# Optimization experiments

Hardware: AMD Instinct MI355X
Metric: run time of the kernel (lower is better)

Reference implementation:

```python
import jax, jax.numpy as jnp
import numpy as np

N, E, IN_DIM, HIDDEN, OUT_DIM, HOPS, NUM_GRAPHS = 50000, 800000, 128, 128, 10, 4, 128


def setup_inputs() -> dict:
    key = jax.random.key(0)
    ks = jax.random.split(key, 10)
    x = jax.random.normal(ks[0], (N, IN_DIM), dtype=jnp.float32)
    edge_index = jax.random.randint(ks[1], (2, E), 0, N, dtype=jnp.int64)
    batch = jnp.sort(jax.random.randint(ks[2], (N,), 0, NUM_GRAPHS, dtype=jnp.int64))
    s = 0.05
    W_in = jax.random.normal(ks[3], (IN_DIM, HIDDEN), dtype=jnp.float32) * s
    b_in = jnp.zeros((HIDDEN,), dtype=jnp.float32)
    W_hops = jax.random.normal(ks[4], (HOPS, HIDDEN, HIDDEN), dtype=jnp.float32) * s
    b_hops = jnp.zeros((HOPS, HIDDEN), dtype=jnp.float32)
    W_cls = jax.random.normal(ks[5], (HIDDEN, OUT_DIM), dtype=jnp.float32) * s
    b_cls = jnp.zeros((OUT_DIM,), dtype=jnp.float32)
    return {"x": x, "edge_index": edge_index, "batch": batch,
            "W_in": W_in, "b_in": b_in, "W_hops": W_hops, "b_hops": b_hops,
            "W_cls": W_cls, "b_cls": b_cls}


def reference(x, edge_index, batch, W_in, b_in, W_hops, b_hops, W_cls, b_cls):
    src, dst = edge_index[0], edge_index[1]
    # LinearEncoder
    h = x @ W_in + b_in
    # GCN symmetric normalization with self-loops (edge weight 1):
    # deg[i] = 1 + in-degree(i)
    deg = 1.0 + jax.ops.segment_sum(jnp.ones((E,), h.dtype), dst, num_segments=N)
    dinv = deg ** -0.5                      # [N]
    edge_norm = (dinv[src] * dinv[dst])[:, None]   # [E,1]
    self_norm = (dinv * dinv)[:, None]             # [N,1]

    def gcn_conv(h, W, b):
        xw = h @ W                                           # [N,H]
        msg = xw[src] * edge_norm                            # gather + scale
        agg = jax.ops.segment_sum(msg, dst, num_segments=N)  # scatter-add
        return agg + xw * self_norm + b

    for i in range(HOPS):
        h = gcn_conv(h, W_hops[i], b_hops[i])
        if i != HOPS - 1:
            h = jax.nn.relu(h)  # dropout is identity in eval mode

    y = h @ W_cls + b_cls                                    # [N,OUT]
    # global mean pool over graphs
    sums = jax.ops.segment_sum(y, batch, num_segments=NUM_GRAPHS)
    cnts = jax.ops.segment_sum(jnp.ones((N,), y.dtype), batch, num_segments=NUM_GRAPHS)
    return sums / jnp.maximum(cnts, 1.0)[:, None]
```

## Files before the change

### kernel.cpp

```cpp
#include <hip/hip_runtime.h>
#include <hip/hip_fp16.h>

#define N_NODES 50000
#define N_EDGES 800000
#define HID 128
#define OUTD 10
#define NGRAPH 128
#define CAP 64
#define OVF_MAX 4096
#define GBM 64
#define EPT 2

typedef __attribute__((ext_vector_type(8))) short short8;
typedef __attribute__((ext_vector_type(4))) float f32x4;

__device__ __forceinline__ int ld_idx(const int* p, int i, int is64) {
  return is64 ? p[2 * i] : p[i];
}

__device__ __forceinline__ void split1(float v, unsigned& hb, unsigned& lb) {
  unsigned u = __float_as_uint(v);
  hb = (u + 0x7FFFu + ((u >> 16) & 1u)) >> 16;
  float r = v - __uint_as_float(hb << 16);
  unsigned ur = __float_as_uint(r);
  lb = (ur + 0x7FFFu + ((ur >> 16) & 1u)) >> 16;
}

__device__ __forceinline__ float4 h4_to_f4(uint2 u) {
  __half2 a = *(__half2*)&u.x;
  __half2 b = *(__half2*)&u.y;
  float2 fa = __half22float2(a);
  float2 fb = __half22float2(b);
  return make_float4(fa.x, fa.y, fb.x, fb.y);
}

__global__ __launch_bounds__(256) void setup_kernel(const int* __restrict__ ei,
                                                    const float* __restrict__ W_in,
                                                    const float* __restrict__ W_hops,
                                                    const float* __restrict__ Wc,
                                                    const float* __restrict__ b4,
                                                    const float* __restrict__ bc,
                                                    int* __restrict__ flag,
                                                    unsigned short* __restrict__ WhiT,
                                                    unsigned short* __restrict__ WloT,
                                                    float* __restrict__ Wf,
                                                    float* __restrict__ bf) {
  int b = blockIdx.x;
  int tid = threadIdx.x;
  if (b == 0) {
    if (tid == 0) {
      int all0 = 1;
      for (int i = 0; i < 64; ++i) {
        if (ei[2 * i + 1] != 0) { all0 = 0; break; }
      }
      flag[0] = all0;
    }
  } else if (b <= 4) {
    int m = b - 1;
    const float* W = (m == 0) ? W_in : (W_hops + (size_t)(m - 1) * HID * HID);
    unsigned short* oh = WhiT + (size_t)m * HID * HID;
    unsigned short* ol = WloT + (size_t)m * HID * HID;
    for (int it = 0; it < 64; ++it) {
      int idx = it * 256 + tid;
      int k = idx >> 7, n = idx & 127;
      unsigned hb, lb;
      split1(W[k * HID + n], hb, lb);
      oh[n * HID + k] = (unsigned short)hb;
      ol[n * HID + k] = (unsigned short)lb;
    }
  } else {
    const float* W4 = W_hops + 3 * (size_t)HID * HID;
    for (int idx = tid; idx < HID * OUTD; idx += 256) {
      int k = idx / OUTD, o = idx % OUTD;
      float s = 0.f;
      for (int j = 0; j < HID; ++j) s += W4[k * HID + j] * Wc[j * OUTD + o];
      Wf[idx] = s;
    }
    if (tid < OUTD) {
      float s = bc[tid];
      for (int j = 0; j < HID; ++j) s += b4[j] * Wc[j * OUTD + tid];
      bf[tid] = s;
    }
  }
}

template <bool A16>
__device__ __forceinline__ void gemm_mfma_body(const void* __restrict__ Av,
                                               const unsigned short* __restrict__ WhT,
                                               const unsigned short* __restrict__ WlT,
                                               const float* __restrict__ bias,
                                               __half* __restrict__ C16,
                                               int M, int row0) {
  __shared__ unsigned short sBall[2 * 64 * HID];
  unsigned short* sBhi = sBall;
  unsigned short* sBlo = sBall + 64 * HID;
  int tid = threadIdx.x;
  int w = tid >> 6, lane = tid & 63;
  int m = lane & 15, kq = lane >> 4;
  int arow = min(row0 + w * 16 + m, M - 1);

  short8 AH[4], AL[4];
#pragma unroll
  for (int kc4 = 0; kc4 < 4; ++kc4) {
    float av[8];
    if (A16) {
      const __half* Ap = (const __half*)Av + (size_t)arow * HID + kq * 8;
      uint4 raw = *(const uint4*)(Ap + kc4 * 32);
      float4 f0 = h4_to_f4(make_uint2(raw.x, raw.y));
      float4 f1 = h4_to_f4(make_uint2(raw.z, raw.w));
      av[0] = f0.x; av[1] = f0.y; av[2] = f0.z; av[3] = f0.w;
      av[4] = f1.x; av[5] = f1.y; av[6] = f1.z; av[7] = f1.w;
    } else {
      const float* Ap = (const float*)Av + (size_t)arow * HID + kq * 8;
      float4 a0 = *(const float4*)(Ap + kc4 * 32);
      float4 a1 = *(const float4*)(Ap + kc4 * 32 + 4);
      av[0] = a0.x; av[1] = a0.y; av[2] = a0.z; av[3] = a0.w;
      av[4] = a1.x; av[5] = a1.y; av[6] = a1.z; av[7] = a1.w;
    }
#pragma unroll
    for (int i = 0; i < 8; ++i) {
      unsigned hb, lb;
      split1(av[i], hb, lb);
      AH[kc4][i] = (short)hb;
      AL[kc4][i] = (short)lb;
    }
  }

  f32x4 acc[8];
#pragma unroll
  for (int j = 0; j < 8; ++j) acc[j] = (f32x4){0.f, 0.f, 0.f, 0.f};

#pragma unroll
  for (int half = 0; half < 2; ++half) {
    if (half) __syncthreads();
#pragma unroll
    for (int it = 0; it < 8; ++it) {
      int f = it * 256 + tid;
      int mat = f >> 10;
      int ln = (f >> 4) & 63;
      int c = f & 15;
      int cs = c ^ (ln & 15);
      const unsigned short* src = (mat ? WlT : WhT) + (size_t)(half * 64 + ln) * HID + c * 8;
      unsigned short* dst = (mat ? sBlo : sBhi) + ln * HID + cs * 8;
      *(uint4*)dst = *(const uint4*)src;
    }
    __syncthreads();

#pragma unroll
    for (int kc4 = 0; kc4 < 4; ++kc4) {
      int kc = kc4 * 4 + kq;
      int cs = kc ^ m;
#pragma unroll
      for (int jl = 0; jl < 4; ++jl) {
        int ln = jl * 16 + m;
        short8 bhi = *(const short8*)&sBhi[ln * HID + cs * 8];
        short8 blo = *(const short8*)&sBlo[ln * HID + cs * 8];
        int j = half * 4 + jl;
        acc[j] = __builtin_amdgcn_mfma_f32_16x16x32_bf16(AH[kc4], bhi, acc[j], 0, 0, 0);
        acc[j] = __builtin_amdgcn_mfma_f32_16x16x32_bf16(AL[kc4], bhi, acc[j], 0, 0, 0);
        acc[j] = __builtin_amdgcn_mfma_f32_16x16x32_bf16(AH[kc4], blo, acc[j], 0, 0, 0);
      }
    }
  }

  __syncthreads();
  float* sC = (float*)sBall;
  int rloc = w * 16 + (lane >> 4) * 4;
#pragma unroll
  for (int j = 0; j < 8; ++j) {
    int col = j * 16 + m;
    float bv = bias ? bias[col] : 0.f;
#pragma unroll
    for (int r = 0; r < 4; ++r)
      sC[(rloc + r) * HID + col] = acc[j][r] + bv;
  }
  __syncthreads();
#pragma unroll
  for (int it = 0; it < 8; ++it) {
    int f = it * 256 + tid;
    int rr = f >> 5;
    int c4 = (f & 31) * 4;
    int grow = row0 + rr;
    if (grow < M) {
      float4 v = *(const float4*)&sC[rr * HID + c4];
      __half2 h0 = __floats2half2_rn(v.x, v.y);
      __half2 h1 = __floats2half2_rn(v.z, v.w);
      uint2 u;
      u.x = *(unsigned*)&h0;
      u.y = *(unsigned*)&h1;
      *(uint2*)(C16 + (size_t)grow * HID + c4) = u;
    }
  }
}

template <bool A16>
__global__ __launch_bounds__(256) void gemm_kernel(const void* __restrict__ A,
                                                   const unsigned short* __restrict__ WhT,
                                                   const unsigned short* __restrict__ WlT,
                                                   __half* __restrict__ C16, int M) {
  gemm_mfma_body<A16>(A, WhT, WlT, nullptr, C16, M, blockIdx.x * GBM);
}

__device__ __forceinline__ void fill_phase(const int* __restrict__ ei,
                                           int* __restrict__ fillcnt,
                                           int* __restrict__ col_fixed,
                                           int* __restrict__ ovf_cnt,
                                           int* __restrict__ ovf,
                                           const int* __restrict__ flag,
                                           int e0, int e1) {
  int is64 = flag[0];
  int tid = threadIdx.x;
  int base = e0 + blockIdx.x * (256 * EPT);
  int dsts[EPT], srcs[EPT], pos[EPT];
#pragma unroll
  for (int u = 0; u < EPT; ++u) {
    int e = base + u * 256 + tid;
    if (e < e1) {
      dsts[u] = ld_idx(ei, N_EDGES + e, is64);
      srcs[u] = ld_idx(ei, e, is64);
    } else {
      dsts[u] = -1; srcs[u] = 0;
    }
  }
#pragma unroll
  for (int u = 0; u < EPT; ++u)
    pos[u] = (dsts[u] >= 0) ? atomicAdd(&fillcnt[dsts[u]], 1) : 0;
#pragma unroll
  for (int u = 0; u < EPT; ++u) {
    if (dsts[u] >= 0) {
      if (pos[u] < CAP) {
        col_fixed[dsts[u] * CAP + pos[u]] = srcs[u];
      } else {
        int o = atomicAdd(ovf_cnt, 1);
        if (o < OVF_MAX) { ovf[2 * o] = dsts[u]; ovf[2 * o + 1] = srcs[u]; }
      }
    }
  }
}

template <bool A16>
__global__ __launch_bounds__(256) void gemm_fill_kernel(const void* __restrict__ A,
                                                        const unsigned short* __restrict__ WhT,
                                                        const unsigned short* __restrict__ WlT,
                                                        const float* __restrict__ bias,
                                                        __half* __restrict__ C16,
                                                        const int* __restrict__ ei,
                                                        int* __restrict__ fillcnt,
                                                        int* __restrict__ col_fixed,
                                                        int* __restrict__ ovf_cnt,
                                                        int* __restrict__ ovf,
                                                        const int* __restrict__ flag,
                                                        int e0, int e1) {
  if (blockIdx.x & 1) {
    fill_phase(ei, fillcnt, col_fixed, ovf_cnt, ovf, flag, e0, e1);
    gemm_mfma_body<A16>(A, WhT, WlT, bias, C16, N_NODES, blockIdx.x * GBM);
  } else {
    gemm_mfma_body<A16>(A, WhT, WlT, bias, C16, N_NODES, blockIdx.x * GBM);
    fill_phase(ei, fillcnt, col_fixed, ovf_cnt, ovf, flag, e0, e1);
  }
}

template <bool FIRST>
__global__ __launch_bounds__(256) void agg_kernel(const __half* __restrict__ xw,
                                                  const int* __restrict__ fillcnt,
                                                  const int* __restrict__ col_fixed,
                                                  float* __restrict__ ew,
                                                  const float* __restrict__ bias,
                                                  const int* __restrict__ ovf_cnt,
                                                  const int* __restrict__ ovf,
                                                  __half* __restrict__ out) {
  int wave = threadIdx.x >> 6;
  int lane = threadIdx.x & 63;
  int node = blockIdx.x * 4 + wave;
  if (node >= N_NODES) return;
  int g = lane >> 4;
  int q = lane & 15;

  const uint4* x4 = (const uint4*)xw;
  int deg = fillcnt[node];
  int m = min(deg, CAP);
  float dd = rsqrtf(1.0f + (float)deg);
  float acc[8];
#pragma unroll
  for (int i = 0; i < 8; ++i) acc[i] = 0.f;

  if (g == 0) {
    float sn = dd * dd;
    uint4 raw = x4[(size_t)node * 16 + q];
    float4 f0 = h4_to_f4(make_uint2(raw.x, raw.y));
    float4 f1 = h4_to_f4(make_uint2(raw.z, raw.w));
    float4 b0 = ((const float4*)bias)[2 * q];
    float4 b1 = ((const float4*)bias)[2 * q + 1];
    acc[0] = f0.x * sn + b0.x; acc[1] = f0.y * sn + b0.y;
    acc[2] = f0.z * sn + b0.z; acc[3] = f0.w * sn + b0.w;
    acc[4] = f1.x * sn + b1.x; acc[5] = f1.y * sn + b1.y;
    acc[6] = f1.z * sn + b1.z; acc[7] = f1.w * sn + b1.w;
  }

  int cidx = node;
  float cw = 0.f;
  if (lane < m) {
    cidx = col_fixed[node * CAP + lane];
    if (FIRST) {
      cw = rsqrtf(1.0f + (float)fillcnt[cidx]) * dd;
      ew[node * CAP + lane] = cw;
    } else {
      cw = ew[node * CAP + lane];
    }
  }

#define GFETCH(JJ, BUF, WB)                                                              \
  {                                                                                      \
    int _sg = min((JJ) + g, 63);                                                         \
    int _src = __builtin_amdgcn_ds_bpermute(_sg << 2, cidx);                             \
    WB = __uint_as_float((unsigned)__builtin_amdgcn_ds_bpermute(_sg << 2,                \
                                                                (int)__float_as_uint(cw))); \
    BUF = x4[(size_t)_src * 16 + q];                                                     \
  }

  if (m > 0) {
    uint4 b0, b1;
    float w0, w1;
    GFETCH(0, b0, w0);
    GFETCH(4, b1, w1);
    for (int jj = 0; jj < m; jj += 4) {
      const __half2* ph = (const __half2*)&b0;
#pragma unroll
      for (int t = 0; t < 4; ++t) {
        float2 f = __half22float2(ph[t]);
        acc[2 * t] = fmaf(f.x, w0, acc[2 * t]);
        acc[2 * t + 1] = fmaf(f.y, w0, acc[2 * t + 1]);
      }
      b0 = b1; w0 = w1;
      GFETCH(jj + 8, b1, w1);
    }
  }
#undef GFETCH

  if (deg > CAP && g == 0) {
    int novf = min(*ovf_cnt, OVF_MAX);
    for (int o = 0; o < novf; ++o) {
      if (ovf[2 * o] == node) {
        int src = ovf[2 * o + 1];
        float w = rsqrtf(1.0f + (float)fillcnt[src]) * dd;
        uint4 raw = x4[(size_t)src * 16 + q];
        const __half2* ph = (const __half2*)&raw;
#pragma unroll
        for (int t = 0; t < 4; ++t) {
          float2 f = __half22float2(ph[t]);
          acc[2 * t] = fmaf(f.x, w, acc[2 * t]);
          acc[2 * t + 1] = fmaf(f.y, w, acc[2 * t + 1]);
        }
      }
    }
  }

#pragma unroll
  for (int i = 0; i < 8; ++i) {
    acc[i] += __shfl_xor(acc[i], 16, 64);
    acc[i] += __shfl_xor(acc[i], 32, 64);
  }

  if (g == 0) {
#pragma unroll
    for (int i = 0; i < 8; ++i) acc[i] = fmaxf(acc[i], 0.f);
    __half2 p0 = __floats2half2_rn(acc[0], acc[1]);
    __half2 p1 = __floats2half2_rn(acc[2], acc[3]);
    __half2 p2 = __floats2half2_rn(acc[4], acc[5]);
    __half2 p3 = __floats2half2_rn(acc[6], acc[7]);
    uint4 u;
    u.x = *(unsigned*)&p0; u.y = *(unsigned*)&p1;
    u.z = *(unsigned*)&p2; u.w = *(unsigned*)&p3;
    ((uint4*)out)[(size_t)node * 16 + q] = u;
  }
}

__global__ __launch_bounds__(256) void z_kernel(const __half* __restrict__ h,
                                                const float* __restrict__ Wf,
                                                float* __restrict__ z, int M) {
  __shared__ float sW[HID * OUTD];
  int tid = threadIdx.x;
  for (int i = tid; i < HID * OUTD; i += 256) sW[i] = Wf[i];
  __syncthreads();
  int row = blockIdx.x * 256 + tid;
  if (row >= M) return;
  float y[OUTD];
#pragma unroll
  for (int o = 0; o < OUTD; ++o) y[o] = 0.f;
  const uint2* hr = (const uint2*)(h + (size_t)row * HID);
  for (int k4 = 0; k4 < 32; ++k4) {
    float4 hv = h4_to_f4(hr[k4]);
    int kb = k4 * 4;
#pragma unroll
    for (int o = 0; o < OUTD; ++o) {
      y[o] += hv.x * sW[(kb + 0) * OUTD + o];
      y[o] += hv.y * sW[(kb + 1) * OUTD + o];
      y[o] += hv.z * sW[(kb + 2) * OUTD + o];
      y[o] += hv.w * sW[(kb + 3) * OUTD + o];
    }
  }
#pragma unroll
  for (int o = 0; o < OUTD; ++o) z[(size_t)row * OUTD + o] = y[o];
}

__global__ __launch_bounds__(256) void agg10_kernel(const float* __restrict__ z,
                                                    const int* __restrict__ fillcnt,
                                                    const int* __restrict__ col_fixed,
                                                    const float* __restrict__ ew,
                                                    const float* __restrict__ bf,
                                                    const int* __restrict__ ovf_cnt,
                                                    const int* __restrict__ ovf,
                                                    const int* __restrict__ batch,
                                                    float* __restrict__ pool,
                                                    float* __restrict__ cnt,
                                                    const int* __restrict__ flag) {
  __shared__ float spool[NGRAPH * OUTD];
  __shared__ float scount[NGRAPH];
  int tid = threadIdx.x;
  for (int i = tid; i < NGRAPH * OUTD; i += 256) spool[i] = 0.f;
  if (tid < NGRAPH) scount[tid] = 0.f;
  __syncthreads();

  int is64 = flag[0];
  int node = blockIdx.x * 256 + tid;
  bool valid = node < N_NODES;
  int nc = valid ? node : (N_NODES - 1);
  int g = ld_idx(batch, nc, is64);

  float acc[OUTD];
#pragma unroll
  for (int o = 0; o < OUTD; ++o) acc[o] = 0.f;
  float c = 0.f;

  if (valid) {
    int deg = fillcnt[node];
    float sn = 1.0f / (1.0f + (float)deg);
#pragma unroll
    for (int o = 0; o < OUTD; ++o) acc[o] = z[(size_t)node * OUTD + o] * sn + bf[o];
    c = 1.f;

    int m = min(deg, CAP);
    for (int j = 0; j < m; ++j) {
      int src = col_fixed[node * CAP + j];
      float w = ew[node * CAP + j];
      const float2* zr = (const float2*)(z + (size_t)src * OUTD);
#pragma unroll
      for (int p = 0; p < 5; ++p) {
        float2 u = zr[p];
        acc[2 * p] += u.x * w;
        acc[2 * p + 1] += u.y * w;
      }
    }
    if (deg > CAP) {
      int novf = min(*ovf_cnt, OVF_MAX);
      float dd = rsqrtf(1.0f + (float)deg);
      for (int o = 0; o < novf; ++o) {
        if (ovf[2 * o] == node) {
          int src = ovf[2 * o + 1];
          float w = rsqrtf(1.0f + (float)fillcnt[src]) * dd;
#pragma unroll
          for (int qq = 0; qq < OUTD; ++qq) acc[qq] += z[(size_t)src * OUTD + qq] * w;
        }
      }
    }
  }

  int g0 = __builtin_amdgcn_readfirstlane(g);
  unsigned long long same = __ballot(g == g0);
  unsigned long long act = __ballot(1);
  if (same == act) {
#pragma unroll
    for (int off = 1; off < 64; off <<= 1) {
#pragma unroll
      for (int o = 0; o < OUTD; ++o) acc[o] += __shfl_xor(acc[o], off, 64);
      c += __shfl_xor(c, off, 64);
    }
    if ((tid & 63) == 0) {
#pragma unroll
      for (int o = 0; o < OUTD; ++o) atomicAdd(&spool[g0 * OUTD + o], acc[o]);
      atomicAdd(&scount[g0], c);
    }
  } else if (valid) {
#pragma unroll
    for (int o = 0; o < OUTD; ++o) atomicAdd(&spool[g * OUTD + o], acc[o]);
    atomicAdd(&scount[g], 1.f);
  }
  __syncthreads();
  for (int i = tid; i < NGRAPH * OUTD; i += 256) {
    float v = spool[i];
    if (v != 0.f) atomicAdd(&pool[i], v);
  }
  if (tid < NGRAPH && scount[tid] != 0.f) atomicAdd(&cnt[tid], scount[tid]);
}

__global__ void finalize_kernel(const float* __restrict__ pool,
                                const float* __restrict__ cnt,
                                float* __restrict__ out) {
  int i = blockIdx.x * blockDim.x + threadIdx.x;
  if (i < NGRAPH * OUTD) {
    float c = cnt[i / OUTD];
    out[i] = pool[i] / fmaxf(c, 1.0f);
  }
}

extern "C" void kernel_launch(void* const* d_in, const int* in_sizes, int n_in,
                              void* d_out, int out_size, void* d_ws, size_t ws_size,
                              hipStream_t stream) {
  const float* x      = (const float*)d_in[0];
  const int*   ei     = (const int*)d_in[1];
  const int*   batch  = (const int*)d_in[2];
  const float* W_in   = (const float*)d_in[3];
  const float* b_in   = (const float*)d_in[4];
  const float* W_hops = (const float*)d_in[5];
  const float* b_hops = (const float*)d_in[6];
  const float* W_cls  = (const float*)d_in[7];
  const float* b_cls  = (const float*)d_in[8];
  float* out = (float*)d_out;

  char* ws = (char*)d_ws;
  size_t off = 0;
  auto alloc = [&](size_t bytes) -> void* {
    void* p = ws + off;
    off += (bytes + 255) & ~(size_t)255;
    return p;
  };

  int*   fillcnt = (int*)alloc(N_NODES * 4);
  int*   ovf_cnt = (int*)alloc(4);
  float* pool    = (float*)alloc(NGRAPH * OUTD * 4);
  float* cnt     = (float*)alloc(NGRAPH * 4);
  size_t zero_bytes = off;
  int*   flag    = (int*)alloc(4);
  int*   ovf     = (int*)alloc(OVF_MAX * 2 * 4);
  int*   col_fixed = (int*)alloc((size_t)N_NODES * CAP * 4);
  float* ew      = (float*)alloc((size_t)N_NODES * CAP * 4);
  __half* bufH   = (__half*)alloc((size_t)N_NODES * HID * 2);
  __half* bufX   = (__half*)alloc((size_t)N_NODES * HID * 2);
  float* z       = (float*)alloc((size_t)N_NODES * OUTD * 4);
  float* Wf      = (float*)alloc(HID * OUTD * 4);
  float* bf      = (float*)alloc(16 * 4);
  unsigned short* WhiT = (unsigned short*)alloc(4 * HID * HID * 2);
  unsigned short* WloT = (unsigned short*)alloc(4 * HID * HID * 2);
  (void)ws_size; (void)in_sizes; (void)n_in; (void)out_size;

  hipMemsetAsync(d_ws, 0, zero_bytes, stream);
  setup_kernel<<<6, 256, 0, stream>>>(ei, W_in, W_hops, W_cls,
                                      b_hops + 3 * HID, b_cls,
                                      flag, WhiT, WloT, Wf, bf);

  const int gblocks = (N_NODES + GBM - 1) / GBM;
  const int ablocks = (N_NODES + 3) / 4;
  const int EHALF = N_EDGES / 2;
  const int WW = HID * HID;

  gemm_fill_kernel<false><<<gblocks, 256, 0, stream>>>(x, WhiT, WloT, b_in, bufH,
                                                       ei, fillcnt, col_fixed, ovf_cnt, ovf,
                                                       flag, 0, EHALF);
  gemm_fill_kernel<true><<<gblocks, 256, 0, stream>>>(bufH, WhiT + WW, WloT + WW, nullptr,
                                                      bufX,
                                                      ei, fillcnt, col_fixed, ovf_cnt, ovf,
                                                      flag, EHALF, N_EDGES);
  agg_kernel<true><<<ablocks, 256, 0, stream>>>(bufX, fillcnt, col_fixed, ew,
                                                b_hops, ovf_cnt, ovf, bufH);
  gemm_kernel<true><<<gblocks, 256, 0, stream>>>(bufH, WhiT + 2 * WW, WloT + 2 * WW,
                                                 bufX, N_NODES);
  agg_kernel<false><<<ablocks, 256, 0, stream>>>(bufX, fillcnt, col_fixed, ew,
                                                 b_hops + HID, ovf_cnt, ovf, bufH);
  gemm_kernel<true><<<gblocks, 256, 0, stream>>>(bufH, WhiT + 3 * WW, WloT + 3 * WW,
                                                 bufX, N_NODES);
  agg_kernel<false><<<ablocks, 256, 0, stream>>>(bufX, fillcnt, col_fixed, ew,
                                                 b_hops + 2 * HID, ovf_cnt, ovf, bufH);
  int nb = (N_NODES + 255) / 256;
  z_kernel<<<nb, 256, 0, stream>>>(bufH, Wf, z, N_NODES);
  agg10_kernel<<<nb, 256, 0, stream>>>(z, fillcnt, col_fixed, ew, bf,
                                       ovf_cnt, ovf, batch, pool, cnt, flag);
  finalize_kernel<<<(NGRAPH * OUTD + 255) / 256, 256, 0, stream>>>(pool, cnt, out);
}
```

Before: 343.8 us.

## Deepen gather prefetch, widen edge fill and z loads, fuse finalize into pooling

Adds a third register buffer to the neighbour-gather prefetch in the aggregation kernel so more loads are in flight per lane. Raises edges per thread in the fill phase and lets blocks with no edges exit early. Widens z_kernel row loads from 8 to 16 bytes. Removes the finalize launch by having the last agg10 block, found through an atomic counter and threadfence, write the normalised mean pool. The deeper prefetch adds register pressure, and the counter adds a grid-wide atomic.

```diff
diff --git a/kernel.cpp b/kernel.cpp
--- a/kernel.cpp
+++ b/kernel.cpp
@@ -9,7 +9,7 @@
 #define CAP 64
 #define OVF_MAX 4096
 #define GBM 64
-#define EPT 2
+#define EPT 4
 
 typedef __attribute__((ext_vector_type(8))) short short8;
 typedef __attribute__((ext_vector_type(4))) float f32x4;
@@ -208,9 +208,10 @@
                                            int* __restrict__ ovf,
                                            const int* __restrict__ flag,
                                            int e0, int e1) {
+  int base = e0 + blockIdx.x * (256 * EPT);
+  if (base >= e1) return;
   int is64 = flag[0];
   int tid = threadIdx.x;
-  int base = e0 + blockIdx.x * (256 * EPT);
   int dsts[EPT], srcs[EPT], pos[EPT];
 #pragma unroll
   for (int u = 0; u < EPT; ++u) {
@@ -319,10 +320,11 @@
   }
 
   if (m > 0) {
-    uint4 b0, b1;
-    float w0, w1;
+    uint4 b0, b1, b2;
+    float w0, w1, w2;
     GFETCH(0, b0, w0);
     GFETCH(4, b1, w1);
+    GFETCH(8, b2, w2);
     for (int jj = 0; jj < m; jj += 4) {
       const __half2* ph = (const __half2*)&b0;
 #pragma unroll
@@ -332,7 +334,8 @@
         acc[2 * t + 1] = fmaf(f.y, w0, acc[2 * t + 1]);
       }
       b0 = b1; w0 = w1;
-      GFETCH(jj + 8, b1, w1);
+      b1 = b2; w1 = w2;
+      GFETCH(jj + 12, b2, w2);
     }
   }
 #undef GFETCH
@@ -387,16 +390,22 @@
   float y[OUTD];
 #pragma unroll
   for (int o = 0; o < OUTD; ++o) y[o] = 0.f;
-  const uint2* hr = (const uint2*)(h + (size_t)row * HID);
-  for (int k4 = 0; k4 < 32; ++k4) {
-    float4 hv = h4_to_f4(hr[k4]);
-    int kb = k4 * 4;
+  const uint4* hr = (const uint4*)(h + (size_t)row * HID);
+  for (int k8 = 0; k8 < 16; ++k8) {
+    uint4 raw = hr[k8];
+    float4 h0 = h4_to_f4(make_uint2(raw.x, raw.y));
+    float4 h1 = h4_to_f4(make_uint2(raw.z, raw.w));
+    int kb = k8 * 8;
 #pragma unroll
     for (int o = 0; o < OUTD; ++o) {
-      y[o] += hv.x * sW[(kb + 0) * OUTD + o];
-      y[o] += hv.y * sW[(kb + 1) * OUTD + o];
-      y[o] += hv.z * sW[(kb + 2) * OUTD + o];
-      y[o] += hv.w * sW[(kb + 3) * OUTD + o];
+      y[o] += h0.x * sW[(kb + 0) * OUTD + o];
+      y[o] += h0.y * sW[(kb + 1) * OUTD + o];
+      y[o] += h0.z * sW[(kb + 2) * OUTD + o];
+      y[o] += h0.w * sW[(kb + 3) * OUTD + o];
+      y[o] += h1.x * sW[(kb + 4) * OUTD + o];
+      y[o] += h1.y * sW[(kb + 5) * OUTD + o];
+      y[o] += h1.z * sW[(kb + 6) * OUTD + o];
+      y[o] += h1.w * sW[(kb + 7) * OUTD + o];
     }
   }
 #pragma unroll
@@ -413,9 +422,12 @@
                                                     const int* __restrict__ batch,
                                                     float* __restrict__ pool,
                                                     float* __restrict__ cnt,
-                                                    const int* __restrict__ flag) {
+                                                    const int* __restrict__ flag,
+                                                    int* __restrict__ done_cnt,
+                                                    float* __restrict__ out) {
   __shared__ float spool[NGRAPH * OUTD];
   __shared__ float scount[NGRAPH];
+  __shared__ int lastflag;
   int tid = threadIdx.x;
   for (int i = tid; i < NGRAPH * OUTD; i += 256) spool[i] = 0.f;
   if (tid < NGRAPH) scount[tid] = 0.f;
@@ -491,15 +503,19 @@
     if (v != 0.f) atomicAdd(&pool[i], v);
   }
   if (tid < NGRAPH && scount[tid] != 0.f) atomicAdd(&cnt[tid], scount[tid]);
-}
-
-__global__ void finalize_kernel(const float* __restrict__ pool,
-                                const float* __restrict__ cnt,
-                                float* __restrict__ out) {
-  int i = blockIdx.x * blockDim.x + threadIdx.x;
-  if (i < NGRAPH * OUTD) {
-    float c = cnt[i / OUTD];
-    out[i] = pool[i] / fmaxf(c, 1.0f);
+
+  __threadfence();
+  if (tid == 0) {
+    int t = atomicAdd(done_cnt, 1);
+    lastflag = (t == (int)gridDim.x - 1);
+  }
+  __syncthreads();
+  if (lastflag) {
+    __threadfence();
+    for (int i = tid; i < NGRAPH * OUTD; i += 256) {
+      float cc = cnt[i / OUTD];
+      out[i] = pool[i] / fmaxf(cc, 1.0f);
+    }
   }
 }
 
@@ -529,6 +545,7 @@
   int*   ovf_cnt = (int*)alloc(4);
   float* pool    = (float*)alloc(NGRAPH * OUTD * 4);
   float* cnt     = (float*)alloc(NGRAPH * 4);
+  int*   done_cnt = (int*)alloc(4);
   size_t zero_bytes = off;
   int*   flag    = (int*)alloc(4);
   int*   ovf     = (int*)alloc(OVF_MAX * 2 * 4);
@@ -573,6 +590,6 @@
   int nb = (N_NODES + 255) / 256;
   z_kernel<<<nb, 256, 0, stream>>>(bufH, Wf, z, N_NODES);
   agg10_kernel<<<nb, 256, 0, stream>>>(z, fillcnt, col_fixed, ew, bf,
-                                       ovf_cnt, ovf, batch, pool, cnt, flag);
-  finalize_kernel<<<(NGRAPH * OUTD + 255) / 256, 256, 0, stream>>>(pool, cnt, out);
-}
+                                       ovf_cnt, ovf, batch, pool, cnt, flag,
+                                       done_cnt, out);
+}
```

After: 345.5 us. About the same (+0.5%).
